# Optimization experiments

Hardware: AMD Instinct MI355X
Metric: run time of the kernel (lower is better)

## Reference

```python
import jax, jax.numpy as jnp
import numpy as np

N = 100_000   # nodes
E = 1_600_000 # edges
IN, HID, OUT = 128, 64, 32


def _glorot(key, fan_in, fan_out):
    s = jnp.sqrt(6.0 / (fan_in + fan_out)).astype(jnp.float32)
    return jax.random.uniform(key, (fan_in, fan_out), jnp.float32, -s, s)


def setup_inputs() -> dict:
    key = jax.random.key(0)
    ks = jax.random.split(key, 8)
    x = jax.random.normal(ks[0], (N, IN), jnp.float32)
    edge_index = jax.random.randint(ks[1], (2, E), 0, N, jnp.int64)
    return {
        "x": x,
        "edge_index": edge_index,
        "W1": _glorot(ks[2], IN, HID),
        "b1": jnp.zeros((HID,), jnp.float32),
        "W_mu": _glorot(ks[3], HID, OUT),
        "b_mu": jnp.zeros((OUT,), jnp.float32),
        "W_ls": _glorot(ks[4], HID, OUT),
        "b_ls": jnp.zeros((OUT,), jnp.float32),
    }


def _gcn_conv(x, W, b, src, dst, n, dinv_sqrt):
    """PyG GCNConv: h = x @ W; symmetric-normalized scatter-add incl. self-loops; + b."""
    h = x @ W                                       # [N, F_out]
    coef = dinv_sqrt[src] * dinv_sqrt[dst]          # [E]
    msg = h[src] * coef[:, None]                    # [E, F_out] gather
    agg = jax.ops.segment_sum(msg, dst, num_segments=n)  # scatter-add
    agg = agg + h * (dinv_sqrt * dinv_sqrt)[:, None]      # self-loop contribution
    return agg + b


def reference(x, edge_index, W1, b1, W_mu, b_mu, W_ls, b_ls):
    src, dst = edge_index[0], edge_index[1]
    n = x.shape[0]
    # degree on graph with self-loops (edge weight 1), shared by all three convs
    deg = jax.ops.segment_sum(jnp.ones((src.shape[0],), x.dtype), dst, num_segments=n) + 1.0
    dinv_sqrt = jax.lax.rsqrt(deg)
    h = jax.nn.relu(_gcn_conv(x, W1, b1, src, dst, n, dinv_sqrt))
    mu = _gcn_conv(h, W_mu, b_mu, src, dst, n, dinv_sqrt)
    logstd = _gcn_conv(h, W_ls, b_ls, src, dst, n, dinv_sqrt)
    return mu, logstd
```

## Files before the change

### kernel.cpp

```cpp
#include <hip/hip_runtime.h>
#include <hip/hip_bf16.h>

#define FIN 128
#define HID 64
#define BSN 128
#define BSHIFT 7
#define SRCBITS 20
#define EPB 4096
#define BSTRIDE 2304
#define STARTBITS 21

typedef __attribute__((ext_vector_type(8))) short short8;
typedef __attribute__((ext_vector_type(4))) float floatx4;

__device__ __forceinline__ float bf2f(unsigned short u) {
    union { unsigned int i; float f; } c;
    c.i = ((unsigned int)u) << 16;
    return c.f;
}

__device__ __forceinline__ unsigned short f2bf(float f) {
    union { float f; unsigned int i; } c;
    c.f = f;
    unsigned int u = c.i;
    unsigned int r = (u + 0x7FFFu + ((u >> 16) & 1u)) >> 16;
    return (unsigned short)r;
}

__global__ void bin_fill(const int* __restrict__ src, const int* __restrict__ dst,
                         int* __restrict__ bcur, unsigned* __restrict__ rec, int E) {
    __shared__ int hist[1024];
    __shared__ int cbase[1024];
    for (int i = threadIdx.x; i < 1024; i += 256) hist[i] = 0;
    __syncthreads();
    int base = blockIdx.x * EPB;
    int lim = min(base + EPB, E);
    for (int e = base + threadIdx.x; e < lim; e += 256)
        atomicAdd(&hist[dst[e] >> BSHIFT], 1);
    __syncthreads();
    for (int b = threadIdx.x; b < 1024; b += 256) {
        int c = hist[b];
        cbase[b] = c ? atomicAdd(&bcur[b], c) : 0;
    }
    __syncthreads();
    for (int i = threadIdx.x; i < 1024; i += 256) hist[i] = 0;
    __syncthreads();
    for (int e = base + threadIdx.x; e < lim; e += 256) {
        int d = dst[e];
        int bkt = d >> BSHIFT;
        int slot = atomicAdd(&hist[bkt], 1);
        rec[bkt * BSTRIDE + cbase[bkt] + slot] =
            (unsigned)src[e] | ((unsigned)(d & (BSN - 1)) << SRCBITS);
    }
}

__global__ void csr_build(const unsigned* __restrict__ rec, const int* __restrict__ bcur,
                          unsigned* __restrict__ rowp, int* __restrict__ csr, int N) {
    __shared__ int cnt[BSN], excl[BSN], cur[BSN];
    int b = blockIdx.x, t = threadIdx.x;
    if (t < BSN) cnt[t] = 0;
    __syncthreads();
    int base = b * BSTRIDE;
    int cb = bcur[b];
    for (int i = t; i < cb; i += 256)
        atomicAdd(&cnt[rec[base + i] >> SRCBITS], 1);
    __syncthreads();
    if (t < BSN) excl[t] = cnt[t];
    __syncthreads();
    for (int off = 1; off < BSN; off <<= 1) {
        int a = 0;
        if (t < BSN && t >= off) a = excl[t - off];
        __syncthreads();
        if (t < BSN) excl[t] += a;
        __syncthreads();
    }
    if (t < BSN) {
        int inc = excl[t];
        int ex = inc - cnt[t];
        excl[t] = ex;
        cur[t] = 0;
        int n = b * BSN + t;
        if (n < N)
            rowp[n] = (unsigned)(base + ex) | ((unsigned)cnt[t] << STARTBITS);
    }
    __syncthreads();
    for (int i = t; i < cb; i += 256) {
        unsigned r = rec[base + i];
        int dl = r >> SRCBITS;
        int slot = atomicAdd(&cur[dl], 1);
        csr[base + excl[dl] + slot] = (int)(r & ((1u << SRCBITS) - 1));
    }
}

__global__ __launch_bounds__(256) void gemm1_mfma(
    const float* __restrict__ x, const float* __restrict__ W1,
    const unsigned* __restrict__ rowp, unsigned short* __restrict__ h0, int N) {
    __shared__ unsigned short Wt[64][136];
    {
        int t = threadIdx.x;
        int k  = t >> 1;
        int c0 = (t & 1) << 5;
        const float* wr = W1 + k * HID + c0;
#pragma unroll
        for (int cc = 0; cc < 32; ++cc)
            Wt[c0 + cc][k] = f2bf(wr[cc]);
    }
    __syncthreads();
    int wave = threadIdx.x >> 6, lane = threadIdx.x & 63;
    int m = lane & 15, q = lane >> 4;
    short8 bfr[4][4];
#pragma unroll
    for (int ct = 0; ct < 4; ++ct)
#pragma unroll
        for (int kk = 0; kk < 4; ++kk)
            bfr[ct][kk] = *((const short8*)&Wt[ct * 16 + m][kk * 32 + q * 8]);
    int ntiles = N >> 4;
    for (int t = blockIdx.x * 4 + wave; t < ntiles; t += gridDim.x * 4) {
        int nbase = t << 4;
        const float* xr = x + (size_t)(nbase + m) * FIN + q * 8;
        short8 afr[4];
#pragma unroll
        for (int kk = 0; kk < 4; ++kk) {
            float4 p0 = *((const float4*)(xr + kk * 32));
            float4 p1 = *((const float4*)(xr + kk * 32 + 4));
            short8 ta;
            ta[0] = (short)f2bf(p0.x); ta[1] = (short)f2bf(p0.y);
            ta[2] = (short)f2bf(p0.z); ta[3] = (short)f2bf(p0.w);
            ta[4] = (short)f2bf(p1.x); ta[5] = (short)f2bf(p1.y);
            ta[6] = (short)f2bf(p1.z); ta[7] = (short)f2bf(p1.w);
            afr[kk] = ta;
        }
        uint4 rp = *((const uint4*)(rowp + nbase + q * 4));
        floatx4 cacc[4];
#pragma unroll
        for (int ct = 0; ct < 4; ++ct) cacc[ct] = floatx4{0.f, 0.f, 0.f, 0.f};
#pragma unroll
        for (int ct = 0; ct < 4; ++ct)
#pragma unroll
            for (int kk = 0; kk < 4; ++kk)
                cacc[ct] = __builtin_amdgcn_mfma_f32_16x16x32_bf16(afr[kk], bfr[ct][kk], cacc[ct], 0, 0, 0);
#pragma unroll
        for (int ct = 0; ct < 4; ++ct) {
#pragma unroll
            for (int r = 0; r < 4; ++r) {
                unsigned pr = (r == 0) ? rp.x : (r == 1) ? rp.y : (r == 2) ? rp.z : rp.w;
                float d = rsqrtf((float)(pr >> STARTBITS) + 1.0f);
                int n = nbase + q * 4 + r;
                h0[(size_t)n * HID + ct * 16 + m] = f2bf(cacc[ct][r] * d);
            }
        }
    }
}


#define ACC8(a, d)                                                      \
    do {                                                                \
        union { unsigned u; float f; } c_;                              \
        c_.u = (d).x << 16;          a[0] += c_.f;                      \
        c_.u = (d).x & 0xFFFF0000u;  a[1] += c_.f;                      \
        c_.u = (d).y << 16;          a[2] += c_.f;                      \
        c_.u = (d).y & 0xFFFF0000u;  a[3] += c_.f;                      \
        c_.u = (d).z << 16;          a[4] += c_.f;                      \
        c_.u = (d).z & 0xFFFF0000u;  a[5] += c_.f;                      \
        c_.u = (d).w << 16;          a[6] += c_.f;                      \
        c_.u = (d).w & 0xFFFF0000u;  a[7] += c_.f;                      \
    } while (0)

__global__ __launch_bounds__(256, 4) void pull(
    const unsigned short* __restrict__ hp,
    const unsigned* __restrict__ rowp,
    const int* __restrict__ csr,
    const float* __restrict__ b1,
    unsigned short* __restrict__ outp, int N, int mode) {
    int lane = threadIdx.x & 63;
    int wave = threadIdx.x >> 6;
    int nd8  = lane >> 3;
    int g    = lane & 7;
    int n = blockIdx.x * 32 + wave * 8 + nd8;
    bool valid = (n < N);
    int nc = valid ? n : 0;
    unsigned rp = rowp[nc];
    int start = (int)(rp & ((1u << STARTBITS) - 1u));
    int deg   = (int)(rp >> STARTBITS);
    int end   = valid ? start + deg : 0;
    if (!valid) start = 0;
    const char* hpb = (const char*)hp;
    unsigned goff = (unsigned)(g << 4);
    uint4 sv = *((const uint4*)(hpb + (((unsigned)nc) << 7) + goff));
    float di = rsqrtf((float)deg + 1.0f);
    float4 bb0 = *((const float4*)(b1 + (g << 3)));
    float4 bb1 = *((const float4*)(b1 + (g << 3) + 4));
    float a[8] = {0.f, 0.f, 0.f, 0.f, 0.f, 0.f, 0.f, 0.f};
    int j = start;
    for (; j + 8 <= end; j += 8) {
        int s0 = csr[j],     s1 = csr[j + 1], s2 = csr[j + 2], s3 = csr[j + 3];
        int s4 = csr[j + 4], s5 = csr[j + 5], s6 = csr[j + 6], s7 = csr[j + 7];
        uint4 d0 = *((const uint4*)(hpb + (((unsigned)s0) << 7) + goff));
        uint4 d1 = *((const uint4*)(hpb + (((unsigned)s1) << 7) + goff));
        uint4 d2 = *((const uint4*)(hpb + (((unsigned)s2) << 7) + goff));
        uint4 d3 = *((const uint4*)(hpb + (((unsigned)s3) << 7) + goff));
        uint4 d4 = *((const uint4*)(hpb + (((unsigned)s4) << 7) + goff));
        uint4 d5 = *((const uint4*)(hpb + (((unsigned)s5) << 7) + goff));
        uint4 d6 = *((const uint4*)(hpb + (((unsigned)s6) << 7) + goff));
        uint4 d7 = *((const uint4*)(hpb + (((unsigned)s7) << 7) + goff));
        ACC8(a, d0); ACC8(a, d1); ACC8(a, d2); ACC8(a, d3);
        ACC8(a, d4); ACC8(a, d5); ACC8(a, d6); ACC8(a, d7);
    }
    if (j + 4 <= end) {
        int s0 = csr[j], s1 = csr[j + 1], s2 = csr[j + 2], s3 = csr[j + 3];
        uint4 d0 = *((const uint4*)(hpb + (((unsigned)s0) << 7) + goff));
        uint4 d1 = *((const uint4*)(hpb + (((unsigned)s1) << 7) + goff));
        uint4 d2 = *((const uint4*)(hpb + (((unsigned)s2) << 7) + goff));
        uint4 d3 = *((const uint4*)(hpb + (((unsigned)s3) << 7) + goff));
        ACC8(a, d0); ACC8(a, d1); ACC8(a, d2); ACC8(a, d3);
        j += 4;
    }
    if (j < end) {
        int i0 = j, i1 = min(j + 1, end - 1), i2 = min(j + 2, end - 1);
        int s0 = csr[i0], s1 = csr[i1], s2 = csr[i2];
        uint4 d0 = *((const uint4*)(hpb + (((unsigned)s0) << 7) + goff));
        uint4 d1 = *((const uint4*)(hpb + (((unsigned)s1) << 7) + goff));
        uint4 d2 = *((const uint4*)(hpb + (((unsigned)s2) << 7) + goff));
        if (j + 1 >= end) { d1.x = 0u; d1.y = 0u; d1.z = 0u; d1.w = 0u; }
        if (j + 2 >= end) { d2.x = 0u; d2.y = 0u; d2.z = 0u; d2.w = 0u; }
        ACC8(a, d0); ACC8(a, d1); ACC8(a, d2);
    }
    if (valid) {
        ACC8(a, sv);
        float v[8];
        if (mode == 0) {
            float t0;
            t0 = di * a[0] + bb0.x; v[0] = (t0 > 0.f ? t0 : 0.f) * di;
            t0 = di * a[1] + bb0.y; v[1] = (t0 > 0.f ? t0 : 0.f) * di;
            t0 = di * a[2] + bb0.z; v[2] = (t0 > 0.f ? t0 : 0.f) * di;
            t0 = di * a[3] + bb0.w; v[3] = (t0 > 0.f ? t0 : 0.f) * di;
            t0 = di * a[4] + bb1.x; v[4] = (t0 > 0.f ? t0 : 0.f) * di;
            t0 = di * a[5] + bb1.y; v[5] = (t0 > 0.f ? t0 : 0.f) * di;
            t0 = di * a[6] + bb1.z; v[6] = (t0 > 0.f ? t0 : 0.f) * di;
            t0 = di * a[7] + bb1.w; v[7] = (t0 > 0.f ? t0 : 0.f) * di;
        } else {
#pragma unroll
            for (int k = 0; k < 8; ++k) v[k] = di * a[k];
        }
        uint4 o;
        o.x = (unsigned)f2bf(v[0]) | ((unsigned)f2bf(v[1]) << 16);
        o.y = (unsigned)f2bf(v[2]) | ((unsigned)f2bf(v[3]) << 16);
        o.z = (unsigned)f2bf(v[4]) | ((unsigned)f2bf(v[5]) << 16);
        o.w = (unsigned)f2bf(v[6]) | ((unsigned)f2bf(v[7]) << 16);
        *((uint4*)(outp + (size_t)n * HID + (g << 3))) = o;
    }
}

__global__ __launch_bounds__(256, 4) void gemm2_mfma(
    const unsigned short* __restrict__ abar,
    const float* __restrict__ Wmu, const float* __restrict__ bmu,
    const float* __restrict__ Wls, const float* __restrict__ bls,
    float* __restrict__ out, int N) {
    int wave = threadIdx.x >> 6, lane = threadIdx.x & 63;
    int m = lane & 15, q = lane >> 4;
    short8 bfr[4][2];
#pragma unroll
    for (int ct = 0; ct < 4; ++ct)
#pragma unroll
        for (int kk = 0; kk < 2; ++kk) {
            short8 tf;
#pragma unroll
            for (int jj = 0; jj < 8; ++jj) {
                int k = kk * 32 + q * 8 + jj;
                int col = ct * 16 + m;
                float w = (col < 32) ? Wmu[k * 32 + col] : Wls[k * 32 + (col - 32)];
                tf[jj] = (short)f2bf(w);
            }
            bfr[ct][kk] = tf;
        }
    float bias[4];
#pragma unroll
    for (int ct = 0; ct < 4; ++ct) {
        int col = ct * 16 + m;
        bias[ct] = (col < 32) ? bmu[col] : bls[col - 32];
    }
    int ntiles = N >> 4;
    int gw = blockIdx.x * 4 + wave;
    int nw = gridDim.x * 4;
    for (int t = gw; t < ntiles; t += nw) {
        int nbase = t << 4;
        const unsigned short* arow = abar + (size_t)(nbase + m) * HID;
        short8 a0 = *((const short8*)(arow + q * 8));
        short8 a1 = *((const short8*)(arow + 32 + q * 8));
        floatx4 cacc[4];
#pragma unroll
        for (int ct = 0; ct < 4; ++ct) cacc[ct] = floatx4{0.f, 0.f, 0.f, 0.f};
#pragma unroll
        for (int ct = 0; ct < 4; ++ct) {
            cacc[ct] = __builtin_amdgcn_mfma_f32_16x16x32_bf16(a0, bfr[ct][0], cacc[ct], 0, 0, 0);
            cacc[ct] = __builtin_amdgcn_mfma_f32_16x16x32_bf16(a1, bfr[ct][1], cacc[ct], 0, 0, 0);
        }
#pragma unroll
        for (int ct = 0; ct < 4; ++ct) {
            int col = ct * 16 + m;
            int which = col >> 5, o = col & 31;
#pragma unroll
            for (int r = 0; r < 4; ++r) {
                int n = nbase + q * 4 + r;
                out[(size_t)which * N * 32 + (size_t)n * 32 + o] = cacc[ct][r] + bias[ct];
            }
        }
    }
}

extern "C" void kernel_launch(void* const* d_in, const int* in_sizes, int n_in,
                              void* d_out, int out_size, void* d_ws, size_t ws_size,
                              hipStream_t stream) {
    const float* x   = (const float*)d_in[0];
    const int*   ei  = (const int*)d_in[1];
    const float* W1  = (const float*)d_in[2];
    const float* b1  = (const float*)d_in[3];
    const float* Wmu = (const float*)d_in[4];
    const float* bmu = (const float*)d_in[5];
    const float* Wls = (const float*)d_in[6];
    const float* bls = (const float*)d_in[7];
    int N = in_sizes[0] / FIN;
    int E = in_sizes[1] / 2;
    const int* src = ei;
    const int* dst = ei + E;
    float* out = (float*)d_out;

    int B = (N + BSN - 1) / BSN;
    int nbin = (E + EPB - 1) / EPB;

    unsigned* rowp = (unsigned*)d_ws;
    int* bcur = (int*)(rowp + N);
    int* csr  = bcur + B;
    unsigned short* bufA = (unsigned short*)(csr + (size_t)B * BSTRIDE);
    char* region2 = (char*)(bufA + (size_t)N * HID);
    unsigned* rec        = (unsigned*)region2;
    unsigned short* bufB = (unsigned short*)region2;

    hipMemsetAsync(bcur, 0, (size_t)B * sizeof(int), stream);
    bin_fill<<<nbin, 256, 0, stream>>>(src, dst, bcur, rec, E);
    csr_build<<<B, 256, 0, stream>>>(rec, bcur, rowp, csr, N);

    gemm1_mfma<<<512, 256, 0, stream>>>(x, W1, rowp, bufA, N);

    int pgrid = (N + 31) / 32;
    pull<<<pgrid, 256, 0, stream>>>(bufA, rowp, csr, b1, bufB, N, 0);
    pull<<<pgrid, 256, 0, stream>>>(bufB, rowp, csr, b1, bufA, N, 1);

    gemm2_mfma<<<512, 256, 0, stream>>>(bufA, Wmu, bmu, Wls, bls, out, N);
}
```

Baseline: 259.8 us.

## Fuse second GEMM into final pull kernel and sort CSR rows by source

The final aggregation pass now stages its 32 aggregated rows in shared memory and runs the 64x64 MFMA output projection in the same block, writing mu/logstd directly. This drops the gemm2 launch and the round trip of the intermediate bf16 buffer. Separately, csr_build now sub-sorts each row's neighbours into 8 coarse source-id ranges, which should improve locality of the gathers. The cost is a larger 1024-entry shared scan in csr_build, plus per-block weight loads and a block barrier in the pull kernel.

After: 256.4 us. About the same (-1.3%).

```diff
diff --git a/kernel.cpp b/kernel.cpp
--- a/kernel.cpp
+++ b/kernel.cpp
@@ -9,6 +9,7 @@
 #define EPB 4096
 #define BSTRIDE 2304
 #define STARTBITS 21
+#define SHSHIFT 14
 
 typedef __attribute__((ext_vector_type(8))) short short8;
 typedef __attribute__((ext_vector_type(4))) float floatx4;
@@ -56,39 +57,47 @@
 
 __global__ void csr_build(const unsigned* __restrict__ rec, const int* __restrict__ bcur,
                           unsigned* __restrict__ rowp, int* __restrict__ csr, int N) {
-    __shared__ int cnt[BSN], excl[BSN], cur[BSN];
+    __shared__ int cnt[1024], inc[1024], cur[1024];
     int b = blockIdx.x, t = threadIdx.x;
-    if (t < BSN) cnt[t] = 0;
+    for (int i = t; i < 1024; i += 256) { cnt[i] = 0; cur[i] = 0; }
     __syncthreads();
     int base = b * BSTRIDE;
     int cb = bcur[b];
-    for (int i = t; i < cb; i += 256)
-        atomicAdd(&cnt[rec[base + i] >> SRCBITS], 1);
-    __syncthreads();
-    if (t < BSN) excl[t] = cnt[t];
-    __syncthreads();
-    for (int off = 1; off < BSN; off <<= 1) {
-        int a = 0;
-        if (t < BSN && t >= off) a = excl[t - off];
+    for (int i = t; i < cb; i += 256) {
+        unsigned r = rec[base + i];
+        int key = (int)((r >> SRCBITS) << 3) | (int)((r & ((1u << SRCBITS) - 1)) >> SHSHIFT);
+        atomicAdd(&cnt[key], 1);
+    }
+    __syncthreads();
+    for (int i = t; i < 1024; i += 256) inc[i] = cnt[i];
+    __syncthreads();
+    for (int off = 1; off < 1024; off <<= 1) {
+        int tmp[4];
+#pragma unroll
+        for (int u = 0; u < 4; ++u) {
+            int i = t + u * 256;
+            tmp[u] = (i >= off) ? inc[i - off] : 0;
+        }
         __syncthreads();
-        if (t < BSN) excl[t] += a;
+#pragma unroll
+        for (int u = 0; u < 4; ++u) inc[t + u * 256] += tmp[u];
         __syncthreads();
     }
     if (t < BSN) {
-        int inc = excl[t];
-        int ex = inc - cnt[t];
-        excl[t] = ex;
-        cur[t] = 0;
+        int kbase = t << 3;
+        int s0 = (kbase == 0) ? 0 : inc[kbase - 1];
+        int deg = inc[kbase + 7] - s0;
         int n = b * BSN + t;
         if (n < N)
-            rowp[n] = (unsigned)(base + ex) | ((unsigned)cnt[t] << STARTBITS);
+            rowp[n] = (unsigned)(base + s0) | ((unsigned)deg << STARTBITS);
     }
     __syncthreads();
     for (int i = t; i < cb; i += 256) {
         unsigned r = rec[base + i];
-        int dl = r >> SRCBITS;
-        int slot = atomicAdd(&cur[dl], 1);
-        csr[base + excl[dl] + slot] = (int)(r & ((1u << SRCBITS) - 1));
+        unsigned s = r & ((1u << SRCBITS) - 1);
+        int key = (int)((r >> SRCBITS) << 3) | (int)(s >> SHSHIFT);
+        int slot = atomicAdd(&cur[key], 1);
+        csr[base + (inc[key] - cnt[key]) + slot] = (int)s;
     }
 }
 
@@ -171,7 +180,11 @@
     const unsigned* __restrict__ rowp,
     const int* __restrict__ csr,
     const float* __restrict__ b1,
-    unsigned short* __restrict__ outp, int N, int mode) {
+    unsigned short* __restrict__ outp,
+    const float* __restrict__ Wmu, const float* __restrict__ bmu,
+    const float* __restrict__ Wls, const float* __restrict__ bls,
+    float* __restrict__ out, int N, int mode) {
+    __shared__ unsigned short ab[32][68];
     int lane = threadIdx.x & 63;
     int wave = threadIdx.x >> 6;
     int nd8  = lane >> 3;
@@ -225,6 +238,7 @@
         if (j + 2 >= end) { d2.x = 0u; d2.y = 0u; d2.z = 0u; d2.w = 0u; }
         ACC8(a, d0); ACC8(a, d1); ACC8(a, d2);
     }
+    uint4 o = {0u, 0u, 0u, 0u};
     if (valid) {
         ACC8(a, sv);
         float v[8];
@@ -242,68 +256,59 @@
 #pragma unroll
             for (int k = 0; k < 8; ++k) v[k] = di * a[k];
         }
-        uint4 o;
         o.x = (unsigned)f2bf(v[0]) | ((unsigned)f2bf(v[1]) << 16);
         o.y = (unsigned)f2bf(v[2]) | ((unsigned)f2bf(v[3]) << 16);
         o.z = (unsigned)f2bf(v[4]) | ((unsigned)f2bf(v[5]) << 16);
         o.w = (unsigned)f2bf(v[6]) | ((unsigned)f2bf(v[7]) << 16);
-        *((uint4*)(outp + (size_t)n * HID + (g << 3))) = o;
-    }
-}
-
-__global__ __launch_bounds__(256, 4) void gemm2_mfma(
-    const unsigned short* __restrict__ abar,
-    const float* __restrict__ Wmu, const float* __restrict__ bmu,
-    const float* __restrict__ Wls, const float* __restrict__ bls,
-    float* __restrict__ out, int N) {
-    int wave = threadIdx.x >> 6, lane = threadIdx.x & 63;
+    }
+    if (mode == 0) {
+        if (valid)
+            *((uint4*)(outp + (size_t)n * HID + (g << 3))) = o;
+        return;
+    }
+    *((uint4*)&ab[wave * 8 + nd8][g << 3]) = o;
+    __syncthreads();
     int m = lane & 15, q = lane >> 4;
-    short8 bfr[4][2];
-#pragma unroll
-    for (int ct = 0; ct < 4; ++ct)
+    int tileId = wave >> 1;
+    int ct0 = (wave & 1) * 2;
+    short8 a0 = *((const short8*)&ab[tileId * 16 + m][q * 8]);
+    short8 a1 = *((const short8*)&ab[tileId * 16 + m][32 + q * 8]);
+    short8 bfr[2][2];
+    float bias[2];
+#pragma unroll
+    for (int c = 0; c < 2; ++c) {
+        int col = (ct0 + c) * 16 + m;
 #pragma unroll
         for (int kk = 0; kk < 2; ++kk) {
             short8 tf;
 #pragma unroll
             for (int jj = 0; jj < 8; ++jj) {
                 int k = kk * 32 + q * 8 + jj;
-                int col = ct * 16 + m;
                 float w = (col < 32) ? Wmu[k * 32 + col] : Wls[k * 32 + (col - 32)];
                 tf[jj] = (short)f2bf(w);
             }
-            bfr[ct][kk] = tf;
-        }
-    float bias[4];
-#pragma unroll
-    for (int ct = 0; ct < 4; ++ct) {
-        int col = ct * 16 + m;
-        bias[ct] = (col < 32) ? bmu[col] : bls[col - 32];
-    }
-    int ntiles = N >> 4;
-    int gw = blockIdx.x * 4 + wave;
-    int nw = gridDim.x * 4;
-    for (int t = gw; t < ntiles; t += nw) {
-        int nbase = t << 4;
-        const unsigned short* arow = abar + (size_t)(nbase + m) * HID;
-        short8 a0 = *((const short8*)(arow + q * 8));
-        short8 a1 = *((const short8*)(arow + 32 + q * 8));
-        floatx4 cacc[4];
-#pragma unroll
-        for (int ct = 0; ct < 4; ++ct) cacc[ct] = floatx4{0.f, 0.f, 0.f, 0.f};
-#pragma unroll
-        for (int ct = 0; ct < 4; ++ct) {
-            cacc[ct] = __builtin_amdgcn_mfma_f32_16x16x32_bf16(a0, bfr[ct][0], cacc[ct], 0, 0, 0);
-            cacc[ct] = __builtin_amdgcn_mfma_f32_16x16x32_bf16(a1, bfr[ct][1], cacc[ct], 0, 0, 0);
-        }
-#pragma unroll
-        for (int ct = 0; ct < 4; ++ct) {
-            int col = ct * 16 + m;
-            int which = col >> 5, o = col & 31;
-#pragma unroll
-            for (int r = 0; r < 4; ++r) {
-                int n = nbase + q * 4 + r;
-                out[(size_t)which * N * 32 + (size_t)n * 32 + o] = cacc[ct][r] + bias[ct];
-            }
+            bfr[c][kk] = tf;
+        }
+        bias[c] = (col < 32) ? bmu[col] : bls[col - 32];
+    }
+    floatx4 cc[2];
+#pragma unroll
+    for (int c = 0; c < 2; ++c) cc[c] = floatx4{0.f, 0.f, 0.f, 0.f};
+#pragma unroll
+    for (int c = 0; c < 2; ++c) {
+        cc[c] = __builtin_amdgcn_mfma_f32_16x16x32_bf16(a0, bfr[c][0], cc[c], 0, 0, 0);
+        cc[c] = __builtin_amdgcn_mfma_f32_16x16x32_bf16(a1, bfr[c][1], cc[c], 0, 0, 0);
+    }
+    int nb = blockIdx.x * 32 + tileId * 16;
+#pragma unroll
+    for (int c = 0; c < 2; ++c) {
+        int col = (ct0 + c) * 16 + m;
+        int which = col >> 5, oc = col & 31;
+#pragma unroll
+        for (int r = 0; r < 4; ++r) {
+            int n2 = nb + q * 4 + r;
+            if (n2 < N)
+                out[(size_t)which * N * 32 + (size_t)n2 * 32 + oc] = cc[c][r] + bias[c];
         }
     }
 }
@@ -343,8 +348,8 @@
     gemm1_mfma<<<512, 256, 0, stream>>>(x, W1, rowp, bufA, N);
 
     int pgrid = (N + 31) / 32;
-    pull<<<pgrid, 256, 0, stream>>>(bufA, rowp, csr, b1, bufB, N, 0);
-    pull<<<pgrid, 256, 0, stream>>>(bufB, rowp, csr, b1, bufA, N, 1);
-
-    gemm2_mfma<<<512, 256, 0, stream>>>(bufA, Wmu, bmu, Wls, bls, out, N);
-}
+    pull<<<pgrid, 256, 0, stream>>>(bufA, rowp, csr, b1, bufB,
+                                    Wmu, bmu, Wls, bls, out, N, 0);
+    pull<<<pgrid, 256, 0, stream>>>(bufB, rowp, csr, b1, (unsigned short*)0,
+                                    Wmu, bmu, Wls, bls, out, N, 1);
+}
```
